# Performance work log

Measured on AMD Instinct MI355X. Metric: run time of the kernel, lower is better.

## Reference

```python
import jax, jax.numpy as jnp
import numpy as np
import math

D_MODEL = 1024
N_HEADS = 16
HEAD_DIM = D_MODEL // N_HEADS
FEAT = 16
WINDOW = 64
EPS_NORM = 1e-6
EPS_LIN = 1e-6
CHUNK = 128


def setup_inputs() -> dict:
    key = jax.random.key(0)
    ks = jax.random.split(key, 7)
    B, T = 2, 2048
    s = 0.02
    return {
        'x': jax.random.normal(ks[0], (B, T, D_MODEL), jnp.float32),
        'norm_w': jnp.ones((D_MODEL,), jnp.float32),
        'Wq': jax.random.normal(ks[1], (D_MODEL, D_MODEL), jnp.float32) * s,
        'Wk': jax.random.normal(ks[2], (D_MODEL, D_MODEL), jnp.float32) * s,
        'Wv': jax.random.normal(ks[3], (D_MODEL, D_MODEL), jnp.float32) * s,
        'Wqf': jax.random.normal(ks[4], (HEAD_DIM, FEAT), jnp.float32) * s,
        'Wkf': jax.random.normal(ks[5], (HEAD_DIM, FEAT), jnp.float32) * s,
        'Wout': jax.random.normal(ks[6], (2 * D_MODEL, D_MODEL), jnp.float32) * s,
    }


def rmsnorm(x, w):
    return x * jax.lax.rsqrt(jnp.mean(x * x, axis=-1, keepdims=True) + EPS_NORM) * w


def taylor_feature_map(x):
    # phi(x) = [1, x, x_i*x_j * (0.5 if i==j else 1/sqrt(2)) for i<=j]
    d = x.shape[-1]
    iu, ju = jnp.triu_indices(d)  # row-major (i, j>=i) matches torch loop order
    scale = jnp.where(iu == ju, 0.5, 1.0 / math.sqrt(2.0)).astype(x.dtype)
    quad = x[..., iu] * x[..., ju] * scale
    ones = jnp.ones(x.shape[:-1] + (1,), dtype=x.dtype)
    return jnp.concatenate([ones, x, quad], axis=-1)  # (..., 1+d+d(d+1)/2)


def linear_attention_causal(q_phi, k_phi, v):
    # Chunked-parallel causal linear attention: y_t = q_t @ KV_t / (q_t @ Ksum_t + eps)
    B, T, H, F = q_phi.shape
    D = v.shape[-1]
    Nc = T // CHUNK
    qc = q_phi.reshape(B, Nc, CHUNK, H, F).transpose(1, 0, 2, 3, 4)  # (Nc,B,C,H,F)
    kc = k_phi.reshape(B, Nc, CHUNK, H, F).transpose(1, 0, 2, 3, 4)
    vc = v.reshape(B, Nc, CHUNK, H, D).transpose(1, 0, 2, 3, 4)      # (Nc,B,C,H,D)
    causal = jnp.tril(jnp.ones((CHUNK, CHUNK), dtype=q_phi.dtype))   # include diagonal

    def step(carry, inp):
        kv, ksum = carry                      # (B,H,F,D), (B,H,F)
        qb, kb, vb = inp
        A = jnp.einsum('bchf,bshf->bhcs', qb, kb) * causal  # intra-chunk quadratic scores
        y = jnp.einsum('bhcs,bshd->bchd', A, vb) + jnp.einsum('bchf,bhfd->bchd', qb, kv)
        z = jnp.einsum('bhcs->bch', A) + jnp.einsum('bchf,bhf->bch', qb, ksum)
        kv = kv + jnp.einsum('bshf,bshd->bhfd', kb, vb)
        ksum = ksum + kb.sum(axis=1)
        return (kv, ksum), y / (z[..., None] + EPS_LIN)

    kv0 = jnp.zeros((B, H, F, D), dtype=q_phi.dtype)
    ks0 = jnp.zeros((B, H, F), dtype=q_phi.dtype)
    _, ys = jax.lax.scan(step, (kv0, ks0), (qc, kc, vc))
    return ys.transpose(1, 0, 2, 3, 4).reshape(B, T, H, D)


def sliding_window_attention(q, k, v):
    B, T, H, D = q.shape
    scale = 1.0 / math.sqrt(D)
    t = jnp.arange(T)
    allowed = (t[None, :] <= t[:, None]) & (t[None, :] >= t[:, None] - WINDOW)  # (T,T)
    scores = jnp.einsum('bqhd,bkhd->bhqk', q, k) * scale
    scores = jnp.where(allowed[None, None], scores, -jnp.inf)
    attn = jax.nn.softmax(scores, axis=-1)
    out = jnp.einsum('bhqk,bkhd->bqhd', attn, v)
    return out.reshape(B, T, H * D)


def reference(x, norm_w, Wq, Wk, Wv, Wqf, Wkf, Wout):
    B, T, _ = x.shape
    h = rmsnorm(x, norm_w)
    q = (h @ Wq).reshape(B, T, N_HEADS, HEAD_DIM)
    k = (h @ Wk).reshape(B, T, N_HEADS, HEAD_DIM)
    v = (h @ Wv).reshape(B, T, N_HEADS, HEAD_DIM)
    q_phi = taylor_feature_map(q @ Wqf)
    k_phi = taylor_feature_map(k @ Wkf)
    lin = linear_attention_causal(q_phi, k_phi, v).reshape(B, T, D_MODEL)
    win = sliding_window_attention(q, k, v)
    out = jnp.concatenate([lin, win], axis=-1) @ Wout
    return x + out
```

## Files before the change

### kernel.cpp

```cpp
#include <hip/hip_runtime.h>
#include <math.h>

#define BB 2
#define TT 2048
#define DM 1024
#define NH 16
#define HD 64
#define FEAT 16
#define WIN 64
#define RTOT (BB*TT)

typedef __bf16 bf16x8 __attribute__((ext_vector_type(8)));
typedef float  f32x4  __attribute__((ext_vector_type(4)));

__device__ __forceinline__ unsigned short f2bf(float f) {
    union { float f; unsigned u; } v; v.f = f;
    unsigned r = v.u + 0x7FFFu + ((v.u >> 16) & 1u);
    return (unsigned short)(r >> 16);
}
__device__ __forceinline__ float bf2f(unsigned short u) {
    union { unsigned u; float f; } v; v.u = ((unsigned)u) << 16; return v.f;
}

__device__ __forceinline__ void gl2lds16(const void* g, void* l) {
    __builtin_amdgcn_global_load_lds(
        (const __attribute__((address_space(1))) void*)g,
        (__attribute__((address_space(3))) void*)l, 16, 0, 0);
}

__global__ __launch_bounds__(256) void rmsnorm_kernel(const float* __restrict__ x,
                                                      const float* __restrict__ w,
                                                      unsigned short* __restrict__ h_bf) {
    int row = blockIdx.x;
    int tid = threadIdx.x;
    const float4* xr = (const float4*)(x + (size_t)row * DM);
    float4 xv = xr[tid];
    float ss = xv.x*xv.x + xv.y*xv.y + xv.z*xv.z + xv.w*xv.w;
    #pragma unroll
    for (int off = 32; off > 0; off >>= 1) ss += __shfl_down(ss, off, 64);
    __shared__ float red[4];
    if ((tid & 63) == 0) red[tid >> 6] = ss;
    __syncthreads();
    float tot = red[0] + red[1] + red[2] + red[3];
    float scale = rsqrtf(tot * (1.0f / DM) + 1e-6f);
    float4 wv = ((const float4*)w)[tid];
    ushort4 o;
    o.x = f2bf(xv.x * scale * wv.x);
    o.y = f2bf(xv.y * scale * wv.y);
    o.z = f2bf(xv.z * scale * wv.z);
    o.w = f2bf(xv.w * scale * wv.w);
    *(ushort4*)&h_bf[(size_t)row * DM + tid * 4] = o;
}

__global__ __launch_bounds__(256) void transpose_bf16_kernel(const float* __restrict__ W0,
                                                             const float* __restrict__ W1,
                                                             const float* __restrict__ W2,
                                                             const float* __restrict__ W3,
                                                             unsigned short* __restrict__ T0,
                                                             unsigned short* __restrict__ T1,
                                                             unsigned short* __restrict__ T2,
                                                             unsigned short* __restrict__ T3) {
    int z = blockIdx.z;
    int K = (z == 3) ? 2048 : 1024;
    const int N = 1024;
    if (blockIdx.y * 64 >= K) return;
    const float* W = (z == 0) ? W0 : (z == 1) ? W1 : (z == 2) ? W2 : W3;
    unsigned short* WT = (z == 0) ? T0 : (z == 1) ? T1 : (z == 2) ? T2 : T3;
    __shared__ float tile[64][65];
    int k0 = blockIdx.y * 64, n0 = blockIdx.x * 64;
    int t = threadIdx.x;
    int r = t >> 4, c4 = (t & 15) * 4;
    #pragma unroll
    for (int i = 0; i < 4; i++) {
        float4 vv = *(const float4*)&W[(size_t)(k0 + r + i*16) * N + n0 + c4];
        tile[r + i*16][c4 + 0] = vv.x;
        tile[r + i*16][c4 + 1] = vv.y;
        tile[r + i*16][c4 + 2] = vv.z;
        tile[r + i*16][c4 + 3] = vv.w;
    }
    __syncthreads();
    int rn = t >> 2, kq = (t & 3) * 16;
    unsigned short u[16];
    #pragma unroll
    for (int i = 0; i < 16; i++) u[i] = f2bf(tile[kq + i][rn]);
    size_t base = (size_t)(n0 + rn) * K + k0 + kq;
    *(uint4*)&WT[base]     = *(uint4*)&u[0];
    *(uint4*)&WT[base + 8] = *(uint4*)&u[8];
}

template<int LD, int NT>
__device__ __forceinline__ void gemm8p_core(const unsigned short* __restrict__ A,
                                            const unsigned short* __restrict__ BT,
                                            unsigned short* __restrict__ Cb,
                                            int k0g) {
    const int N = 1024;
    __shared__ __align__(16) unsigned short L[2][4][256 * 32];
    int tid = threadIdx.x;
    int lane = tid & 63;
    int w = tid >> 6;
    int wm = (w >> 2) * 128, wn = (w & 3) * 64;
    int m0 = blockIdx.y * 256, n0 = blockIdx.x * 256;
    int hi = lane >> 4;
    int l15 = lane & 15;

    int c0 = tid, c1 = tid + 512;
    int r0 = c0 >> 2, kh0 = ((c0 & 3) - (r0 >> 1)) & 3;
    int r1 = c1 >> 2, kh1 = ((c1 & 3) - (r1 >> 1)) & 3;
    const unsigned short* aS0 = A  + (size_t)(m0 + r0) * LD + k0g + kh0 * 8;
    const unsigned short* aS1 = A  + (size_t)(m0 + r1) * LD + k0g + kh1 * 8;
    const unsigned short* bS0 = BT + (size_t)(n0 + r0) * LD + k0g + kh0 * 8;
    const unsigned short* bS1 = BT + (size_t)(n0 + r1) * LD + k0g + kh1 * 8;

    int aoff[8], boff[4];
    #pragma unroll
    for (int i = 0; i < 8; i++) {
        int m = wm + i * 16 + l15;
        aoff[i] = m * 32 + (((hi + (m >> 1)) & 3) * 8);
    }
    #pragma unroll
    for (int j = 0; j < 4; j++) {
        int n = wn + j * 16 + l15;
        boff[j] = n * 32 + (((hi + (n >> 1)) & 3) * 8);
    }

    f32x4 acc[8][4];
    #pragma unroll
    for (int i = 0; i < 8; i++)
        #pragma unroll
        for (int j = 0; j < 4; j++)
            acc[i][j] = (f32x4){0.f, 0.f, 0.f, 0.f};

#define STG8(kt, bf, rg) do {                                         \
        int _go = (kt) * 64 + ((rg) >> 1) * 32;                       \
        unsigned short* _d = &L[bf][rg][0];                           \
        if ((rg) & 1) { gl2lds16(bS0 + _go, _d + c0 * 8);             \
                        gl2lds16(bS1 + _go, _d + c1 * 8); }           \
        else          { gl2lds16(aS0 + _go, _d + c0 * 8);             \
                        gl2lds16(aS1 + _go, _d + c1 * 8); }           \
    } while (0)

    STG8(0, 0, 0); STG8(0, 0, 1); STG8(0, 0, 2); STG8(0, 0, 3);
    asm volatile("s_waitcnt vmcnt(4)" ::: "memory");
    __builtin_amdgcn_s_barrier();

    for (int t = 0; t < NT; t++) {
        int rd = t & 1, st = rd ^ 1;
        bool stg = (t + 1 < NT);
        const unsigned short* A0 = &L[rd][0][0];
        const unsigned short* B0 = &L[rd][1][0];
        const unsigned short* A1 = &L[rd][2][0];
        const unsigned short* B1 = &L[rd][3][0];
        bf16x8 af[4], bfr[4];

        #pragma unroll
        for (int i = 0; i < 4; i++) af[i] = *(const bf16x8*)&A0[aoff[i]];
        #pragma unroll
        for (int j = 0; j < 4; j++) bfr[j] = *(const bf16x8*)&B0[boff[j]];
        if (stg) STG8(t + 1, st, 0);
        __builtin_amdgcn_s_barrier();
        __builtin_amdgcn_s_setprio(1);
        #pragma unroll
        for (int i = 0; i < 4; i++)
            #pragma unroll
            for (int j = 0; j < 4; j++)
                acc[i][j] = __builtin_amdgcn_mfma_f32_16x16x32_bf16(af[i], bfr[j], acc[i][j], 0, 0, 0);
        __builtin_amdgcn_s_setprio(0);
        __builtin_amdgcn_s_barrier();

        #pragma unroll
        for (int i = 0; i < 4; i++) af[i] = *(const bf16x8*)&A0[aoff[4 + i]];
        if (stg) {
            STG8(t + 1, st, 1);
            asm volatile("s_waitcnt vmcnt(4)" ::: "memory");
        } else {
            asm volatile("s_waitcnt vmcnt(0)" ::: "memory");
        }
        __builtin_amdgcn_s_barrier();
        __builtin_amdgcn_s_setprio(1);
        #pragma unroll
        for (int i = 0; i < 4; i++)
            #pragma unroll
            for (int j = 0; j < 4; j++)
                acc[4 + i][j] = __builtin_amdgcn_mfma_f32_16x16x32_bf16(af[i], bfr[j], acc[4 + i][j], 0, 0, 0);
        __builtin_amdgcn_s_setprio(0);
        __builtin_amdgcn_s_barrier();

        #pragma unroll
        for (int i = 0; i < 4; i++) af[i] = *(const bf16x8*)&A1[aoff[i]];
        #pragma unroll
        for (int j = 0; j < 4; j++) bfr[j] = *(const bf16x8*)&B1[boff[j]];
        if (stg) STG8(t + 1, st, 2);
        __builtin_amdgcn_s_barrier();
        __builtin_amdgcn_s_setprio(1);
        #pragma unroll
        for (int i = 0; i < 4; i++)
            #pragma unroll
            for (int j = 0; j < 4; j++)
                acc[i][j] = __builtin_amdgcn_mfma_f32_16x16x32_bf16(af[i], bfr[j], acc[i][j], 0, 0, 0);
        __builtin_amdgcn_s_setprio(0);
        __builtin_amdgcn_s_barrier();

        #pragma unroll
        for (int i = 0; i < 4; i++) af[i] = *(const bf16x8*)&A1[aoff[4 + i]];
        if (stg) {
            STG8(t + 1, st, 3);
            asm volatile("s_waitcnt vmcnt(4)" ::: "memory");
        }
        __builtin_amdgcn_s_barrier();
        __builtin_amdgcn_s_setprio(1);
        #pragma unroll
        for (int i = 0; i < 4; i++)
            #pragma unroll
            for (int j = 0; j < 4; j++)
                acc[4 + i][j] = __builtin_amdgcn_mfma_f32_16x16x32_bf16(af[i], bfr[j], acc[4 + i][j], 0, 0, 0);
        __builtin_amdgcn_s_setprio(0);
        __builtin_amdgcn_s_barrier();
    }
#undef STG8

    #pragma unroll
    for (int i = 0; i < 8; i++) {
        #pragma unroll
        for (int j = 0; j < 4; j++) {
            int col = n0 + wn + j * 16 + l15;
            #pragma unroll
            for (int r = 0; r < 4; r++) {
                int row = m0 + wm + i * 16 + hi * 4 + r;
                Cb[(size_t)row * N + col] = f2bf(acc[i][j][r]);
            }
        }
    }
}

__global__ __launch_bounds__(512, 2) void gemm_qkv_mfma(const unsigned short* __restrict__ A,
                                                        const unsigned short* __restrict__ BT0,
                                                        const unsigned short* __restrict__ BT1,
                                                        const unsigned short* __restrict__ BT2,
                                                        unsigned short* __restrict__ C0,
                                                        unsigned short* __restrict__ C1,
                                                        unsigned short* __restrict__ C2) {
    const unsigned short* BT = (blockIdx.z == 0) ? BT0 : (blockIdx.z == 1) ? BT1 : BT2;
    unsigned short* C = (blockIdx.z == 0) ? C0 : (blockIdx.z == 1) ? C1 : C2;
    gemm8p_core<1024, 16>(A, BT, C, 0);
}

__global__ __launch_bounds__(512, 2) void gemm_out_mfma(const unsigned short* __restrict__ A,
                                                        const unsigned short* __restrict__ BT,
                                                        unsigned short* __restrict__ P0,
                                                        unsigned short* __restrict__ P1,
                                                        unsigned short* __restrict__ P2,
                                                        unsigned short* __restrict__ P3) {
    unsigned short* P = (blockIdx.z == 0) ? P0 : (blockIdx.z == 1) ? P1
                      : (blockIdx.z == 2) ? P2 : P3;
    gemm8p_core<2048, 8>(A, BT, P, blockIdx.z * 512);
}

__global__ __launch_bounds__(256) void out_reduce_kernel(const float* __restrict__ x,
                                                         const unsigned short* __restrict__ P0,
                                                         const unsigned short* __restrict__ P1,
                                                         const unsigned short* __restrict__ P2,
                                                         const unsigned short* __restrict__ P3,
                                                         float* __restrict__ out) {
    int g = blockIdx.x * 256 + threadIdx.x;
    size_t e = (size_t)g * 4;
    float4 xv = *(const float4*)&x[e];
    ushort4 a = *(const ushort4*)&P0[e];
    ushort4 b = *(const ushort4*)&P1[e];
    ushort4 c = *(const ushort4*)&P2[e];
    ushort4 d = *(const ushort4*)&P3[e];
    float4 o;
    o.x = xv.x + bf2f(a.x) + bf2f(b.x) + bf2f(c.x) + bf2f(d.x);
    o.y = xv.y + bf2f(a.y) + bf2f(b.y) + bf2f(c.y) + bf2f(d.y);
    o.z = xv.z + bf2f(a.z) + bf2f(b.z) + bf2f(c.z) + bf2f(d.z);
    o.w = xv.w + bf2f(a.w) + bf2f(b.w) + bf2f(c.w) + bf2f(d.w);
    *(float4*)&out[e] = o;
}

__global__ __launch_bounds__(256) void feat_kernel(const unsigned short* __restrict__ qb,
                                                   const unsigned short* __restrict__ kb,
                                                   const float* __restrict__ Wqf,
                                                   const float* __restrict__ Wkf,
                                                   unsigned short* __restrict__ qf,
                                                   unsigned short* __restrict__ kf) {
    __shared__ float Wl[HD * FEAT];
    const unsigned short* src = blockIdx.z ? kb : qb;
    const float* Wm = blockIdx.z ? Wkf : Wqf;
    unsigned short* dst = blockIdx.z ? kf : qf;
    int tid = threadIdx.x;
    ((float4*)Wl)[tid] = ((const float4*)Wm)[tid];
    __syncthreads();
    int gid = blockIdx.x * 256 + tid;
    int f = gid & 15;
    int rowh = gid >> 4;
    const unsigned short* s = src + (size_t)rowh * HD;
    float acc = 0.f;
    #pragma unroll
    for (int d = 0; d < HD; d++) acc += bf2f(s[d]) * Wl[d * FEAT + f];
    dst[gid] = f2bf(acc);
}

__global__ __launch_bounds__(256) void win_mfma_kernel(const unsigned short* __restrict__ q_bf,
                                                       const unsigned short* __restrict__ k_bf,
                                                       const unsigned short* __restrict__ v_bf,
                                                       unsigned short* __restrict__ cat_bf) {
    int qtile = blockIdx.x;
    int bh = blockIdx.y;
    int h = bh & 15;
    int b = bh >> 4;
    int tid = threadIdx.x;
    int lane = tid & 63;
    int wv = tid >> 6;
    int qr0 = wv * 16;
    int t0 = qtile * 64;
    int k0 = t0 - 64;

    __shared__ __align__(16) unsigned short Qs[64 * 64];
    __shared__ __align__(16) unsigned short Ks[128 * 64];
    __shared__ __align__(16) unsigned short Vt[64 * 128];
    __shared__ __align__(16) unsigned short Pl[64 * 128];

    #pragma unroll
    for (int half = 0; half < 2; half++) {
        int slot = tid + half * 256;
        int row = slot >> 3, pos = slot & 7;
        int o = (pos - row) & 7;
        gl2lds16(q_bf + (size_t)(b * TT + t0 + row) * (NH * HD) + h * HD + o * 8,
                 &Qs[slot * 8]);
    }
    #pragma unroll
    for (int qd = 0; qd < 4; qd++) {
        int slot = tid + qd * 256;
        int row = slot >> 3, pos = slot & 7;
        int o = (pos - row) & 7;
        int kg = k0 + row;
        if (kg >= 0) {
            gl2lds16(k_bf + (size_t)(b * TT + kg) * (NH * HD) + h * HD + o * 8,
                     &Ks[slot * 8]);
        } else {
            uint4 z = {0, 0, 0, 0};
            *(uint4*)&Ks[slot * 8] = z;
        }
    }
    {
        int kk = tid & 127;
        int dh = tid >> 7;
        int kg = k0 + kk;
        unsigned short tmp[32];
        if (kg >= 0) {
            size_t base = (size_t)(b * TT + kg) * (NH * HD) + h * HD + dh * 32;
            *(uint4*)&tmp[0]  = *(const uint4*)&v_bf[base];
            *(uint4*)&tmp[8]  = *(const uint4*)&v_bf[base + 8];
            *(uint4*)&tmp[16] = *(const uint4*)&v_bf[base + 16];
            *(uint4*)&tmp[24] = *(const uint4*)&v_bf[base + 24];
        } else {
            #pragma unroll
            for (int d = 0; d < 32; d++) tmp[d] = 0;
        }
        int o = kk >> 3, klow = kk & 7;
        #pragma unroll
        for (int d = 0; d < 32; d++) {
            int dim = dh * 32 + d;
            Vt[dim * 128 + ((o + dim) & 15) * 8 + klow] = tmp[d];
        }
    }
    __syncthreads();

    int hi = lane >> 4;
    int lan15 = lane & 15;
    f32x4 sc[8];
    #pragma unroll
    for (int nt = 0; nt < 8; nt++) sc[nt] = (f32x4){0.f, 0.f, 0.f, 0.f};
    #pragma unroll
    for (int ks = 0; ks < 2; ks++) {
        int m = qr0 + lan15;
        int oA = ks * 4 + hi;
        bf16x8 a = *(const bf16x8*)&Qs[m * 64 + ((oA + m) & 7) * 8];
        #pragma unroll
        for (int nt = 0; nt < 8; nt++) {
            int n = nt * 16 + lan15;
            bf16x8 bb = *(const bf16x8*)&Ks[n * 64 + ((oA + n) & 7) * 8];
            sc[nt] = __builtin_amdgcn_mfma_f32_16x16x32_bf16(a, bb, sc[nt], 0, 0, 0);
        }
    }

    float lrow[4];
    #pragma unroll
    for (int r = 0; r < 4; r++) {
        int tq = t0 + qr0 + hi * 4 + r;
        float mx = -1e30f;
        #pragma unroll
        for (int nt = 0; nt < 8; nt++) {
            int s = k0 + nt * 16 + lan15;
            bool ok = (s >= 0) && (s <= tq) && (s >= tq - WIN);
            float vv = ok ? sc[nt][r] * 0.125f : -1e30f;
            sc[nt][r] = vv;
            mx = fmaxf(mx, vv);
        }
        #pragma unroll
        for (int off = 1; off < 16; off <<= 1) mx = fmaxf(mx, __shfl_xor(mx, off, 64));
        float ls = 0.f;
        #pragma unroll
        for (int nt = 0; nt < 8; nt++) {
            float e = __expf(sc[nt][r] - mx);
            sc[nt][r] = e;
            ls += e;
        }
        #pragma unroll
        for (int off = 1; off < 16; off <<= 1) ls += __shfl_xor(ls, off, 64);
        lrow[r] = ls;
    }

    #pragma unroll
    for (int nt = 0; nt < 8; nt++) {
        #pragma unroll
        for (int r = 0; r < 4; r++) {
            int row = qr0 + hi * 4 + r;
            int col = nt * 16 + lan15;
            Pl[row * 128 + (((col >> 3) + row) & 15) * 8 + (col & 7)] = f2bf(sc[nt][r]);
        }
    }
    __syncthreads();

    f32x4 y[4];
    #pragma unroll
    for (int nt = 0; nt < 4; nt++) y[nt] = (f32x4){0.f, 0.f, 0.f, 0.f};
    #pragma unroll
    for (int ks = 0; ks < 4; ks++) {
        int m = qr0 + lan15;
        int oA = ks * 4 + hi;
        bf16x8 a = *(const bf16x8*)&Pl[m * 128 + ((oA + m) & 15) * 8];
        #pragma unroll
        for (int nt = 0; nt < 4; nt++) {
            int n = nt * 16 + lan15;
            bf16x8 bb = *(const bf16x8*)&Vt[n * 128 + ((oA + n) & 15) * 8];
            y[nt] = __builtin_amdgcn_mfma_f32_16x16x32_bf16(a, bb, y[nt], 0, 0, 0);
        }
    }

    #pragma unroll
    for (int nt = 0; nt < 4; nt++) {
        #pragma unroll
        for (int r = 0; r < 4; r++) {
            int row = qr0 + hi * 4 + r;
            int dim = nt * 16 + lan15;
            cat_bf[(size_t)(b * TT + t0 + row) * (2 * DM) + DM + h * HD + dim] =
                f2bf(y[nt][r] / lrow[r]);
        }
    }
}

#define PHI 160
#define NCH 32
#define KVROWS 65
#define CH_STRIDE ((size_t)32 * KVROWS * PHI)

__global__ __launch_bounds__(256) void lin_kv_kernel(const unsigned short* __restrict__ kf,
                                                     const unsigned short* __restrict__ v_bf,
                                                     unsigned short* __restrict__ kvbuf) {
    int c = blockIdx.x, bh = blockIdx.y;
    int h = bh & 15, b = bh >> 4;
    int tid = threadIdx.x, lane = tid & 63, w = tid >> 6;
    int hi = lane >> 4, l15 = lane & 15;

    __shared__ unsigned short kf_l[64 * 16];
    __shared__ __align__(16) unsigned short PhiT[192 * 76];
    __shared__ __align__(16) unsigned short Vt[80 * 64];
    __shared__ unsigned short iu[136], ju[136];
    __shared__ float sclut[136];

    if (tid < 136) {
        int qq = tid, i = 0;
        while (qq >= 16 - i) { qq -= 16 - i; i++; }
        iu[tid] = (unsigned short)i; ju[tid] = (unsigned short)(i + qq);
        sclut[tid] = (qq == 0) ? 0.5f : 0.70710678118654752f;
    }
    {
        int r = tid >> 2, f4 = (tid & 3) * 4;
        *(ushort4*)&kf_l[r * 16 + f4] =
            *(const ushort4*)&kf[((size_t)((b * TT + c * 64 + r) * NH + h)) * FEAT + f4];
    }
    {
        int p = tid & 31, dq = (tid >> 5) * 8;
        size_t base0 = ((size_t)(b * TT + c * 64 + 2 * p)) * DM + h * HD + dq;
        unsigned short a[8], bq[8];
        *(uint4*)a  = *(const uint4*)&v_bf[base0];
        *(uint4*)bq = *(const uint4*)&v_bf[base0 + DM];
        int colo = p >> 2, coll = (2 * p) & 7;
        #pragma unroll
        for (int d = 0; d < 8; d++) {
            int row = dq + d;
            ushort2 u; u.x = a[d]; u.y = bq[d];
            *(ushort2*)&Vt[row * 64 + ((colo + row) & 7) * 8 + coll] = u;
        }
        #pragma unroll
        for (int i = 0; i < 4; i++) {
            int e = tid + i * 256;
            Vt[(64 + (e >> 6)) * 64 + (e & 63)] = 0x3F80;
        }
    }
    __syncthreads();
    {
        int s = tid & 63, fb = tid >> 6;
        const unsigned short* krow = &kf_l[s * 16];
        for (int it = 0; it < 40; it++) {
            int f = fb * 40 + it;
            float val;
            if (f == 0) val = 1.f;
            else if (f < 17) val = bf2f(krow[f - 1]);
            else if (f < 153) { int qq = f - 17; val = bf2f(krow[iu[qq]]) * bf2f(krow[ju[qq]]) * sclut[qq]; }
            else val = 0.f;
            PhiT[f * 76 + s] = f2bf(val);
        }
    }
    __syncthreads();
    f32x4 acc[5][3];
    #pragma unroll
    for (int m = 0; m < 5; m++)
        #pragma unroll
        for (int j = 0; j < 3; j++) acc[m][j] = (f32x4){0.f, 0.f, 0.f, 0.f};
    #pragma unroll
    for (int ks = 0; ks < 2; ks++) {
        bf16x8 bfrag[3];
        #pragma unroll
        for (int j = 0; j < 3; j++)
            bfrag[j] = *(const bf16x8*)&PhiT[((3 * w + j) * 16 + l15) * 76 + ks * 32 + hi * 8];
        #pragma unroll
        for (int m = 0; m < 5; m++) {
            int mrow = m * 16 + l15;
            bf16x8 afrag = *(const bf16x8*)&Vt[mrow * 64 + (((ks * 4 + hi) + mrow) & 7) * 8];
            #pragma unroll
            for (int j = 0; j < 3; j++)
                acc[m][j] = __builtin_amdgcn_mfma_f32_16x16x32_bf16(afrag, bfrag[j], acc[m][j], 0, 0, 0);
        }
    }
    size_t obase = ((size_t)c * 32 + bh) * (KVROWS * PHI);
    #pragma unroll
    for (int m = 0; m < 5; m++) {
        #pragma unroll
        for (int j = 0; j < 3; j++) {
            int f = (3 * w + j) * 16 + l15;
            if (f >= PHI) continue;
            #pragma unroll
            for (int r = 0; r < 4; r++) {
                int row = m * 16 + hi * 4 + r;
                if (row >= KVROWS) continue;
                kvbuf[obase + row * PHI + f] = f2bf(acc[m][j][r]);
            }
        }
    }
}

__global__ __launch_bounds__(256) void lin_scan_kernel(unsigned short* __restrict__ kvbuf) {
    int e = blockIdx.x * 256 + threadIdx.x;
    int bh = blockIdx.y;
    if (e >= KVROWS * PHI) return;
    float acc = 0.f;
    size_t off = (size_t)bh * (KVROWS * PHI) + e;
    for (int c = 0; c < NCH; c++) {
        float vv = bf2f(kvbuf[off]);
        kvbuf[off] = f2bf(acc);
        acc += vv;
        off += CH_STRIDE;
    }
}

__global__ __launch_bounds__(256) void lin_out_kernel(const unsigned short* __restrict__ qf,
                                                      const unsigned short* __restrict__ kf,
                                                      const unsigned short* __restrict__ v_bf,
                                                      const unsigned short* __restrict__ kvbuf,
                                                      unsigned short* __restrict__ cat_bf) {
    int c = blockIdx.x, bh = blockIdx.y;
    int h = bh & 15, b = bh >> 4;
    int tid = threadIdx.x, lane = tid & 63, w = tid >> 6;
    int hi = lane >> 4, l15 = lane & 15;

    __shared__ unsigned short qf_l[64 * 16];
    __shared__ __align__(16) unsigned short kf_lb[64 * 34];
    __shared__ __align__(16) unsigned short KVS_l[80 * 164];
    __shared__ __align__(16) unsigned short Vt[80 * 64];
    __shared__ __align__(16) unsigned short Phi_l[64 * 164];
    __shared__ __align__(16) unsigned short P_l[64 * 64];
    __shared__ unsigned short iu[136], ju[136];
    __shared__ float sclut[136];

    if (tid < 136) {
        int qq = tid, i = 0;
        while (qq >= 16 - i) { qq -= 16 - i; i++; }
        iu[tid] = (unsigned short)i; ju[tid] = (unsigned short)(i + qq);
        sclut[tid] = (qq == 0) ? 0.5f : 0.70710678118654752f;
    }
    {
        int r = tid >> 2, f4 = (tid & 3) * 4;
        *(ushort4*)&qf_l[r * 16 + f4] =
            *(const ushort4*)&qf[((size_t)((b * TT + c * 64 + r) * NH + h)) * FEAT + f4];
    }
    {
        int r = tid >> 2, f4 = (tid & 3) * 4;
        *(ushort4*)&kf_lb[r * 34 + f4] =
            *(const ushort4*)&kf[((size_t)((b * TT + c * 64 + r) * NH + h)) * FEAT + f4];
        ushort4 z4 = {0, 0, 0, 0};
        *(ushort4*)&kf_lb[r * 34 + 16 + f4] = z4;
    }
    {
        int p = tid & 31, dq = (tid >> 5) * 8;
        size_t base0 = ((size_t)(b * TT + c * 64 + 2 * p)) * DM + h * HD + dq;
        unsigned short a[8], bq[8];
        *(uint4*)a  = *(const uint4*)&v_bf[base0];
        *(uint4*)bq = *(const uint4*)&v_bf[base0 + DM];
        int colo = p >> 2, coll = (2 * p) & 7;
        #pragma unroll
        for (int d = 0; d < 8; d++) {
            int row = dq + d;
            ushort2 u; u.x = a[d]; u.y = bq[d];
            *(ushort2*)&Vt[row * 64 + ((colo + row) & 7) * 8 + coll] = u;
        }
        #pragma unroll
        for (int i = 0; i < 4; i++) {
            int e = tid + i * 256;
            Vt[(64 + (e >> 6)) * 64 + (e & 63)] = 0x3F80;
        }
    }
    {
        size_t gbase = ((size_t)c * 32 + bh) * (KVROWS * PHI);
        #pragma unroll
        for (int i = 0; i < 11; i++) {
            int e4 = tid + i * 256;
            if (e4 < KVROWS * 40) {
                int r = e4 / 40, q4 = (e4 % 40) * 4;
                *(ushort4*)&KVS_l[r * 164 + q4] =
                    *(const ushort4*)&kvbuf[gbase + r * PHI + q4];
            }
        }
        #pragma unroll
        for (int i = 0; i < 3; i++) {
            int e4 = tid + i * 256;
            if (e4 < 15 * 40) {
                int r = 65 + e4 / 40, q4 = (e4 % 40) * 4;
                ushort4 z4 = {0, 0, 0, 0};
                *(ushort4*)&KVS_l[r * 164 + q4] = z4;
            }
        }
    }
    __syncthreads();

    {
        int s = tid & 63, fb = tid >> 6;
        const unsigned short* qrow = &qf_l[s * 16];
        for (int it = 0; it < 40; it++) {
            int f = fb * 40 + it;
            float val;
            if (f == 0) val = 1.f;
            else if (f < 17) val = bf2f(qrow[f - 1]);
            else if (f < 153) { int qq = f - 17; val = bf2f(qrow[iu[qq]]) * bf2f(qrow[ju[qq]]) * sclut[qq]; }
            else val = 0.f;
            Phi_l[s * 164 + f] = f2bf(val);
        }
    }
    __syncthreads();

    f32x4 acc[5];
    #pragma unroll
    for (int n = 0; n < 5; n++) acc[n] = (f32x4){0.f, 0.f, 0.f, 0.f};

    int t_m = w * 16 + l15;

    #pragma unroll
    for (int ks = 0; ks < 5; ks++) {
        bf16x8 af = *(const bf16x8*)&Phi_l[t_m * 164 + ks * 32 + hi * 8];
        #pragma unroll
        for (int n = 0; n < 5; n++) {
            bf16x8 bb = *(const bf16x8*)&KVS_l[(n * 16 + l15) * 164 + ks * 32 + hi * 8];
            acc[n] = __builtin_amdgcn_mfma_f32_16x16x32_bf16(af, bb, acc[n], 0, 0, 0);
        }
    }

    {
        union { unsigned short u[8]; bf16x8 v; } aq;
        #pragma unroll
        for (int j = 0; j < 8; j++) {
            int f = hi * 8 + j;
            aq.u[j] = (f < 16) ? qf_l[t_m * 16 + f] : (unsigned short)0;
        }
        #pragma unroll
        for (int n = 0; n < 4; n++) {
            bf16x8 bk = *(const bf16x8*)&kf_lb[(n * 16 + l15) * 34 + hi * 8];
            f32x4 zv = {0.f, 0.f, 0.f, 0.f};
            f32x4 sc = __builtin_amdgcn_mfma_f32_16x16x32_bf16(aq.v, bk, zv, 0, 0, 0);
            int sl = n * 16 + l15;
            #pragma unroll
            for (int r = 0; r < 4; r++) {
                int rl = w * 16 + hi * 4 + r;
                float sv = 1.f + 0.5f * sc[r];
                sv = sv * sv;
                if (sl > rl) sv = 0.f;
                P_l[rl * 64 + (((sl >> 3) + rl) & 7) * 8 + (sl & 7)] = f2bf(sv);
            }
        }
    }
    __syncthreads();

    #pragma unroll
    for (int ks = 0; ks < 2; ks++) {
        int oA = ks * 4 + hi;
        bf16x8 a = *(const bf16x8*)&P_l[t_m * 64 + ((oA + t_m) & 7) * 8];
        #pragma unroll
        for (int n = 0; n < 5; n++) {
            int nrow = n * 16 + l15;
            bf16x8 bb = *(const bf16x8*)&Vt[nrow * 64 + ((oA + nrow) & 7) * 8];
            acc[n] = __builtin_amdgcn_mfma_f32_16x16x32_bf16(a, bb, acc[n], 0, 0, 0);
        }
    }

    #pragma unroll
    for (int r = 0; r < 4; r++) {
        float zz = __shfl(acc[4][r], (lane & 48), 64);
        int token = c * 64 + w * 16 + hi * 4 + r;
        #pragma unroll
        for (int n = 0; n < 4; n++) {
            int d = n * 16 + l15;
            cat_bf[((size_t)(b * TT + token)) * (2 * DM) + h * HD + d] =
                f2bf(acc[n][r] / (zz + 1e-6f));
        }
    }
}

extern "C" void kernel_launch(void* const* d_in, const int* in_sizes, int n_in,
                              void* d_out, int out_size, void* d_ws, size_t ws_size,
                              hipStream_t stream) {
    const float* x      = (const float*)d_in[0];
    const float* norm_w = (const float*)d_in[1];
    const float* Wq     = (const float*)d_in[2];
    const float* Wk     = (const float*)d_in[3];
    const float* Wv     = (const float*)d_in[4];
    const float* Wqf    = (const float*)d_in[5];
    const float* Wkf    = (const float*)d_in[6];
    const float* Wout   = (const float*)d_in[7];
    float* out = (float*)d_out;

    char* p = (char*)d_ws;
    unsigned short* h_bf = (unsigned short*)p; p += (size_t)RTOT * DM * 2;
    unsigned short* WqT  = (unsigned short*)p; p += (size_t)DM * DM * 2;
    unsigned short* WkT  = (unsigned short*)p; p += (size_t)DM * DM * 2;
    unsigned short* WvT  = (unsigned short*)p; p += (size_t)DM * DM * 2;
    unsigned short* WoT  = (unsigned short*)p; p += (size_t)DM * 2 * DM * 2;
    unsigned short* q_bf = (unsigned short*)p; p += (size_t)RTOT * DM * 2;
    unsigned short* k_bf = (unsigned short*)p; p += (size_t)RTOT * DM * 2;
    unsigned short* v_bf = (unsigned short*)p; p += (size_t)RTOT * DM * 2;
    unsigned short* qf_bf = (unsigned short*)p; p += (size_t)RTOT * NH * FEAT * 2;
    unsigned short* kf_bf = (unsigned short*)p; p += (size_t)RTOT * NH * FEAT * 2;
    unsigned short* cat_bf = (unsigned short*)p; p += (size_t)RTOT * 2 * DM * 2;
    unsigned short* kvbuf  = (unsigned short*)p; p += (size_t)NCH * 32 * KVROWS * PHI * 2;
    unsigned short* P0 = (unsigned short*)p; p += (size_t)RTOT * DM * 2;
    unsigned short* P1 = (unsigned short*)p; p += (size_t)RTOT * DM * 2;
    unsigned short* P2 = h_bf;
    unsigned short* P3 = q_bf;

    rmsnorm_kernel<<<RTOT, 256, 0, stream>>>(x, norm_w, h_bf);
    transpose_bf16_kernel<<<dim3(16, 32, 4), 256, 0, stream>>>(Wq, Wk, Wv, Wout, WqT, WkT, WvT, WoT);
    gemm_qkv_mfma<<<dim3(4, 16, 3), 512, 0, stream>>>(h_bf, WqT, WkT, WvT, q_bf, k_bf, v_bf);
    feat_kernel<<<dim3((RTOT * NH * FEAT) / 256, 1, 2), 256, 0, stream>>>(q_bf, k_bf, Wqf, Wkf, qf_bf, kf_bf);
    win_mfma_kernel<<<dim3(TT / 64, BB * NH), 256, 0, stream>>>(q_bf, k_bf, v_bf, cat_bf);
    lin_kv_kernel<<<dim3(NCH, BB * NH), 256, 0, stream>>>(kf_bf, v_bf, kvbuf);
    lin_scan_kernel<<<dim3((KVROWS * PHI + 255) / 256, BB * NH), 256, 0, stream>>>(kvbuf);
    lin_out_kernel<<<dim3(NCH, BB * NH), 256, 0, stream>>>(qf_bf, kf_bf, v_bf, kvbuf, cat_bf);
    gemm_out_mfma<<<dim3(4, 16, 4), 512, 0, stream>>>(cat_bf, WoT, P0, P1, P2, P3);
    out_reduce_kernel<<<RTOT * DM / 1024, 256, 0, stream>>>(x, P0, P1, P2, P3, out);
}
```

Baseline: 254.1 us.

## Restructure GEMM main loop from eight phases into two half-K phases

The MFMA GEMM inner loop drops from eight barrier-separated phases per K-tile to two. Each phase now loads all eight A fragments and four B fragments, issues two staging copies at once, and runs 32 MFMAs. Fewer s_barrier calls and longer uninterrupted MFMA runs per phase are meant to cut sync overhead. The cost is more live registers (8 A fragments) under the 512-thread, 2-block launch bound, and less interleaving of global-to-LDS copies with compute, which could cause register pressure or stalls.

```diff
diff --git a/kernel.cpp b/kernel.cpp
--- a/kernel.cpp
+++ b/kernel.cpp
@@ -89,7 +89,7 @@
 }
 
 template<int LD, int NT>
-__device__ __forceinline__ void gemm8p_core(const unsigned short* __restrict__ A,
+__device__ __forceinline__ void gemm2h_core(const unsigned short* __restrict__ A,
                                             const unsigned short* __restrict__ BT,
                                             unsigned short* __restrict__ Cb,
                                             int k0g) {
@@ -150,71 +150,45 @@
         const unsigned short* B0 = &L[rd][1][0];
         const unsigned short* A1 = &L[rd][2][0];
         const unsigned short* B1 = &L[rd][3][0];
-        bf16x8 af[4], bfr[4];
-
-        #pragma unroll
-        for (int i = 0; i < 4; i++) af[i] = *(const bf16x8*)&A0[aoff[i]];
+        bf16x8 af[8], bfr[4];
+
+        asm volatile("" ::: "memory");
+        #pragma unroll
+        for (int i = 0; i < 8; i++) af[i] = *(const bf16x8*)&A0[aoff[i]];
         #pragma unroll
         for (int j = 0; j < 4; j++) bfr[j] = *(const bf16x8*)&B0[boff[j]];
-        if (stg) STG8(t + 1, st, 0);
-        __builtin_amdgcn_s_barrier();
+        if (stg) { STG8(t + 1, st, 0); STG8(t + 1, st, 1); }
         __builtin_amdgcn_s_setprio(1);
         #pragma unroll
-        for (int i = 0; i < 4; i++)
+        for (int i = 0; i < 8; i++)
             #pragma unroll
             for (int j = 0; j < 4; j++)
                 acc[i][j] = __builtin_amdgcn_mfma_f32_16x16x32_bf16(af[i], bfr[j], acc[i][j], 0, 0, 0);
         __builtin_amdgcn_s_setprio(0);
-        __builtin_amdgcn_s_barrier();
-
-        #pragma unroll
-        for (int i = 0; i < 4; i++) af[i] = *(const bf16x8*)&A0[aoff[4 + i]];
         if (stg) {
-            STG8(t + 1, st, 1);
             asm volatile("s_waitcnt vmcnt(4)" ::: "memory");
         } else {
             asm volatile("s_waitcnt vmcnt(0)" ::: "memory");
         }
         __builtin_amdgcn_s_barrier();
+
+        asm volatile("" ::: "memory");
+        #pragma unroll
+        for (int i = 0; i < 8; i++) af[i] = *(const bf16x8*)&A1[aoff[i]];
+        #pragma unroll
+        for (int j = 0; j < 4; j++) bfr[j] = *(const bf16x8*)&B1[boff[j]];
+        if (stg) { STG8(t + 1, st, 2); STG8(t + 1, st, 3); }
         __builtin_amdgcn_s_setprio(1);
         #pragma unroll
-        for (int i = 0; i < 4; i++)
-            #pragma unroll
-            for (int j = 0; j < 4; j++)
-                acc[4 + i][j] = __builtin_amdgcn_mfma_f32_16x16x32_bf16(af[i], bfr[j], acc[4 + i][j], 0, 0, 0);
-        __builtin_amdgcn_s_setprio(0);
-        __builtin_amdgcn_s_barrier();
-
-        #pragma unroll
-        for (int i = 0; i < 4; i++) af[i] = *(const bf16x8*)&A1[aoff[i]];
-        #pragma unroll
-        for (int j = 0; j < 4; j++) bfr[j] = *(const bf16x8*)&B1[boff[j]];
-        if (stg) STG8(t + 1, st, 2);
-        __builtin_amdgcn_s_barrier();
-        __builtin_amdgcn_s_setprio(1);
-        #pragma unroll
-        for (int i = 0; i < 4; i++)
+        for (int i = 0; i < 8; i++)
             #pragma unroll
             for (int j = 0; j < 4; j++)
                 acc[i][j] = __builtin_amdgcn_mfma_f32_16x16x32_bf16(af[i], bfr[j], acc[i][j], 0, 0, 0);
         __builtin_amdgcn_s_setprio(0);
-        __builtin_amdgcn_s_barrier();
-
-        #pragma unroll
-        for (int i = 0; i < 4; i++) af[i] = *(const bf16x8*)&A1[aoff[4 + i]];
         if (stg) {
-            STG8(t + 1, st, 3);
             asm volatile("s_waitcnt vmcnt(4)" ::: "memory");
-        }
-        __builtin_amdgcn_s_barrier();
-        __builtin_amdgcn_s_setprio(1);
-        #pragma unroll
-        for (int i = 0; i < 4; i++)
-            #pragma unroll
-            for (int j = 0; j < 4; j++)
-                acc[4 + i][j] = __builtin_amdgcn_mfma_f32_16x16x32_bf16(af[i], bfr[j], acc[4 + i][j], 0, 0, 0);
-        __builtin_amdgcn_s_setprio(0);
-        __builtin_amdgcn_s_barrier();
+            __builtin_amdgcn_s_barrier();
+        }
     }
 #undef STG8
 
@@ -241,7 +215,7 @@
                                                         unsigned short* __restrict__ C2) {
     const unsigned short* BT = (blockIdx.z == 0) ? BT0 : (blockIdx.z == 1) ? BT1 : BT2;
     unsigned short* C = (blockIdx.z == 0) ? C0 : (blockIdx.z == 1) ? C1 : C2;
-    gemm8p_core<1024, 16>(A, BT, C, 0);
+    gemm2h_core<1024, 16>(A, BT, C, 0);
 }
 
 __global__ __launch_bounds__(512, 2) void gemm_out_mfma(const unsigned short* __restrict__ A,
@@ -252,7 +226,7 @@
                                                         unsigned short* __restrict__ P3) {
     unsigned short* P = (blockIdx.z == 0) ? P0 : (blockIdx.z == 1) ? P1
                       : (blockIdx.z == 2) ? P2 : P3;
-    gemm8p_core<2048, 8>(A, BT, P, blockIdx.z * 512);
+    gemm2h_core<2048, 8>(A, BT, P, blockIdx.z * 512);
 }
 
 __global__ __launch_bounds__(256) void out_reduce_kernel(const float* __restrict__ x,
```

Result: no change. 250.2 us (-1.6%).
